# Kernel optimization log

Hardware: AMD Instinct MI355X
Metric: run time of the kernel (lower is better)

## Reference

```python
import jax, jax.numpy as jnp
import numpy as np

EPS = 1e-5
GROUPS = 8


def setup_inputs() -> dict:
    key = jax.random.key(0)
    ks = jax.random.split(key, 3)
    b, c, h, w = 8, 256, 64, 64
    x = jax.random.normal(ks[0], (b, c, h, w), dtype=jnp.float32)
    # 1x1 convs are just channel matmuls; store weights as [out_ch, in_ch]
    qkv_w = jax.random.normal(ks[1], (3 * c, c), dtype=jnp.float32) * (c ** -0.5)
    qkv_b = jnp.zeros((3 * c,), dtype=jnp.float32)
    out_w = jax.random.normal(ks[2], (c, c), dtype=jnp.float32) * (c ** -0.5)
    out_b = jnp.zeros((c,), dtype=jnp.float32)
    gn_w = jnp.ones((c,), dtype=jnp.float32)
    gn_b = jnp.zeros((c,), dtype=jnp.float32)
    return {"x": x, "gn_w": gn_w, "gn_b": gn_b, "qkv_w": qkv_w,
            "qkv_b": qkv_b, "out_w": out_w, "out_b": out_b}


def _group_norm(x, gn_w, gn_b):
    # x: [b, c, h, w]; normalize per (group, sample) over (c//g, h, w)
    b, c, h, w = x.shape
    xg = x.reshape(b, GROUPS, c // GROUPS, h * w)
    mean = xg.mean(axis=(2, 3), keepdims=True)
    var = xg.var(axis=(2, 3), keepdims=True)
    xn = (xg - mean) * jax.lax.rsqrt(var + EPS)
    xn = xn.reshape(b, c, h * w)
    return xn * gn_w[None, :, None] + gn_b[None, :, None]


def reference(x, gn_w, gn_b, qkv_w, qkv_b, out_w, out_b):
    b, c, h, w = x.shape
    scale = 1.0 / np.sqrt(c).astype(np.float32)  # matches channels ** -0.5
    nx = _group_norm(x, gn_w, gn_b)                       # [b, c, n]
    qkv = jnp.einsum('oc,bcn->bon', qkv_w, nx) + qkv_b[None, :, None]
    q, k, v = qkv[:, :c], qkv[:, c:2 * c], qkv[:, 2 * c:]  # each [b, c, n]
    attn = jnp.einsum('bci,bcj->bij', q, k) * scale        # [b, n, n]
    attn = jax.nn.softmax(attn, axis=-1)
    out = jnp.einsum('bij,bcj->bci', attn, v)              # [b, c, n]
    out = jnp.einsum('oc,bcn->bon', out_w, out) + out_b[None, :, None]
    return out.reshape(b, c, h, w) + x
```

## Files before the change

kernel.cpp:

```cpp
#include <hip/hip_runtime.h>
#include <math.h>


#define Bn 8
#define Cn 256
#define HWn 4096
#define Gn 8
#define CPGn 32
#define Mqkv 768
#define EPSf 1e-5f
#define QSCALEf 0.0625f
#define RTHR 8.0f

typedef short bf16x8 __attribute__((ext_vector_type(8)));
typedef float f32x4 __attribute__((ext_vector_type(4)));

__device__ __forceinline__ unsigned short f2bf(float f) {
  union { float f; unsigned u; } v; v.f = f;
  unsigned r = v.u + 0x7FFFu + ((v.u >> 16) & 1u);
  return (unsigned short)(r >> 16);
}

__device__ __forceinline__ int cvt_pk_bf16(float lo, float hi) {
  int d;
  asm("v_cvt_pk_bf16_f32 %0, %1, %2" : "=v"(d) : "v"(lo), "v"(hi));
  return d;
}

__global__ __launch_bounds__(1024)
void gn_stats_kernel(const float* __restrict__ x, const float* __restrict__ gn_w,
                     const float* __restrict__ gn_b, float* __restrict__ s_out,
                     float* __restrict__ t_out) {
  const int b = blockIdx.x / Gn, g = blockIdx.x % Gn;
  const float4* base = (const float4*)(x + ((size_t)(b * Cn + g * CPGn)) * HWn);
  const int n4 = CPGn * HWn / 4;
  float sum = 0.f, sq = 0.f;
  for (int i = threadIdx.x; i < n4; i += 1024) {
    float4 v = base[i];
    sum += (v.x + v.y) + (v.z + v.w);
    sq  += (v.x * v.x + v.y * v.y) + (v.z * v.z + v.w * v.w);
  }
  __shared__ float ss[1024], s2[1024];
  ss[threadIdx.x] = sum; s2[threadIdx.x] = sq;
  __syncthreads();
  for (int off = 512; off > 0; off >>= 1) {
    if ((int)threadIdx.x < off) {
      ss[threadIdx.x] += ss[threadIdx.x + off];
      s2[threadIdx.x] += s2[threadIdx.x + off];
    }
    __syncthreads();
  }
  if (threadIdx.x < CPGn) {
    const float inv_n = 1.f / (float)(CPGn * HWn);
    float mean = ss[0] * inv_n;
    float var  = s2[0] * inv_n - mean * mean;
    float rstd = rsqrtf(var + EPSf);
    int c = g * CPGn + (int)threadIdx.x;
    float sc = gn_w[c] * rstd;
    s_out[b * Cn + c] = sc;
    t_out[b * Cn + c] = gn_b[c] - mean * sc;
  }
}

__global__ __launch_bounds__(256)
void qkv_gemm_kernel(const float* __restrict__ x, const float* __restrict__ w,
                     const float* __restrict__ wb, const float* __restrict__ s_aff,
                     const float* __restrict__ t_aff, unsigned short* __restrict__ Qt,
                     unsigned short* __restrict__ Kt, unsigned short* __restrict__ Vb) {
  const int b = blockIdx.z;
  const int m0 = blockIdx.y * 64, n0 = blockIdx.x * 64;
  const int tid = threadIdx.x, tx = tid & 15, ty = tid >> 4;
  __shared__ float As[16][68];
  __shared__ float Bs[16][68];
  const float* xb = x + (size_t)b * Cn * HWn;
  const float* sb = s_aff + b * Cn;
  const float* tb = t_aff + b * Cn;
  float acc[4][4] = {};
  const int am = tid >> 2, ak = (tid & 3) * 4;
  const int bk = tid >> 4, bn = (tid & 15) * 4;
  for (int k0 = 0; k0 < Cn; k0 += 16) {
    {
      float4 a = *(const float4*)(w + (size_t)(m0 + am) * Cn + (k0 + ak));
      As[ak + 0][am] = a.x; As[ak + 1][am] = a.y; As[ak + 2][am] = a.z; As[ak + 3][am] = a.w;
      int c = k0 + bk;
      float4 v = *(const float4*)(xb + (size_t)c * HWn + (n0 + bn));
      float sc = sb[c], sh = tb[c];
      Bs[bk][bn + 0] = v.x * sc + sh; Bs[bk][bn + 1] = v.y * sc + sh;
      Bs[bk][bn + 2] = v.z * sc + sh; Bs[bk][bn + 3] = v.w * sc + sh;
    }
    __syncthreads();
#pragma unroll
    for (int kk = 0; kk < 16; ++kk) {
      float4 av = *(const float4*)&As[kk][ty * 4];
      float4 bv = *(const float4*)&Bs[kk][tx * 4];
      float aa[4] = {av.x, av.y, av.z, av.w};
      float bb[4] = {bv.x, bv.y, bv.z, bv.w};
#pragma unroll
      for (int i2 = 0; i2 < 4; ++i2)
#pragma unroll
        for (int j2 = 0; j2 < 4; ++j2)
          acc[i2][j2] = fmaf(aa[i2], bb[j2], acc[i2][j2]);
    }
    __syncthreads();
  }
  float bias[4];
#pragma unroll
  for (int i2 = 0; i2 < 4; ++i2) bias[i2] = wb[m0 + ty * 4 + i2];

  if (m0 < 512) {
    unsigned short* dst = (m0 < 256) ? Qt : Kt;
    const float scl = (m0 < 256) ? QSCALEf : 1.0f;
    const int cbase = (m0 & 255) + ty * 4;
#pragma unroll
    for (int j2 = 0; j2 < 4; ++j2) {
      int n = n0 + tx * 4 + j2;
      ushort4 pk;
      pk.x = f2bf((acc[0][j2] + bias[0]) * scl);
      pk.y = f2bf((acc[1][j2] + bias[1]) * scl);
      pk.z = f2bf((acc[2][j2] + bias[2]) * scl);
      pk.w = f2bf((acc[3][j2] + bias[3]) * scl);
      *(ushort4*)(dst + ((size_t)(b * HWn + n) * Cn + cbase)) = pk;
    }
  } else {
#pragma unroll
    for (int i2 = 0; i2 < 4; ++i2) {
      int c = (m0 - 512) + ty * 4 + i2;
      ushort4 pk;
      pk.x = f2bf(acc[i2][0] + bias[i2]);
      pk.y = f2bf(acc[i2][1] + bias[i2]);
      pk.z = f2bf(acc[i2][2] + bias[i2]);
      pk.w = f2bf(acc[i2][3] + bias[i2]);
      *(ushort4*)(Vb + ((size_t)(b * Cn + c) * HWn + n0 + tx * 4)) = pk;
    }
  }
}

__global__ __launch_bounds__(256, 2)
void attn_kernel(const unsigned short* __restrict__ Qt,
                 const unsigned short* __restrict__ Kt,
                 const unsigned short* __restrict__ Vb,
                 float* __restrict__ outp) {
  const int bid = blockIdx.x;
  const int b = bid & 7, i0 = (bid >> 3) * 64;
  const int tid = threadIdx.x;
  const int wv = tid >> 6, l = tid & 63;
  const int l15 = l & 15, lq = l >> 4;

  __shared__ unsigned short Ks[8192];
  __shared__ unsigned short Vs[8192];
  char* KsB = (char*)Ks;
  char* VsB = (char*)Vs;

  const unsigned short* Qb = Qt + ((size_t)b * HWn + i0) * Cn;
  const unsigned short* Kb = Kt + (size_t)b * HWn * Cn;
  const unsigned short* Vg = Vb + (size_t)b * Cn * HWn;

  bf16x8 qf[8];
  {
    const unsigned short* qrow = Qb + (size_t)(wv * 16 + l15) * Cn + lq * 8;
#pragma unroll
    for (int kc = 0; kc < 8; ++kc) qf[kc] = *(const bf16x8*)(qrow + kc * 32);
  }

  const int jk = ((tid >> 6) & 1) * 16 + (tid & 15);
  const int ck = (tid >> 7) * 32 + ((tid >> 4) & 3) * 8;
  const int cv = (tid >> 6) * 16 + (tid & 15);
  const int jv = ((tid >> 4) & 3) * 8;
  const unsigned short* gK = Kb + (size_t)jk * Cn + ck;
  const unsigned short* gV = Vg + (size_t)cv * HWn + jv;

  const int laneA = l15 + ((lq & 1) << 5);
  const int laneB = laneA + 16;
  const int shi = lq >> 1;

  bf16x8 kst[4], vst[4];
#pragma unroll
  for (int q = 0; q < 4; ++q) kst[q] = *(const bf16x8*)(gK + q * 64);
#pragma unroll
  for (int q = 0; q < 4; ++q) vst[q] = *(const bf16x8*)(gV + (size_t)q * 64 * HWn);
  gK += 32 * Cn; gV += 32;

  f32x4 o_acc[16];
#pragma unroll
  for (int cs = 0; cs < 16; ++cs) o_acc[cs] = (f32x4)(0.f);
  float m_i = -INFINITY, l_i = 0.f;

#pragma unroll 1
  for (int t = 0; t < 128; ++t) {
#pragma unroll
    for (int q = 0; q < 4; ++q) *(bf16x8*)(KsB + tid * 16 + q * 4096) = kst[q];
#pragma unroll
    for (int q = 0; q < 4; ++q) *(bf16x8*)(VsB + tid * 16 + q * 4096) = vst[q];
    __syncthreads();
    if (t < 127) {
#pragma unroll
      for (int q = 0; q < 4; ++q) kst[q] = *(const bf16x8*)(gK + q * 64);
#pragma unroll
      for (int q = 0; q < 4; ++q) vst[q] = *(const bf16x8*)(gV + (size_t)q * 64 * HWn);
      gK += 32 * Cn; gV += 32;
    }

    f32x4 s0 = (f32x4)(0.f), s1 = (f32x4)(0.f);
#pragma unroll
    for (int kc = 0; kc < 8; ++kc) {
      bf16x8 kf0 = *(const bf16x8*)(KsB + l * 16 + kc * 2048);
      bf16x8 kf1 = *(const bf16x8*)(KsB + l * 16 + kc * 2048 + 1024);
      s0 = __builtin_amdgcn_mfma_f32_16x16x32_bf16(kf0, qf[kc], s0, 0, 0, 0);
      s1 = __builtin_amdgcn_mfma_f32_16x16x32_bf16(kf1, qf[kc], s1, 0, 0, 0);
    }

    float p[2][4];
#pragma unroll
    for (int r = 0; r < 4; ++r) { p[0][r] = s0[r]; p[1][r] = s1[r]; }
    float rm = fmaxf(fmaxf(fmaxf(p[0][0], p[0][1]), fmaxf(p[0][2], p[0][3])),
                     fmaxf(fmaxf(p[1][0], p[1][1]), fmaxf(p[1][2], p[1][3])));
    rm = fmaxf(rm, __shfl_xor(rm, 16));
    rm = fmaxf(rm, __shfl_xor(rm, 32));
    if (!__all(rm - m_i <= RTHR)) {
      float mn = fmaxf(m_i, rm);
      float alpha = __expf(m_i - mn);
      m_i = mn;
      l_i *= alpha;
      float a0 = __shfl(alpha, 4 * lq + 0);
      float a1 = __shfl(alpha, 4 * lq + 1);
      float a2 = __shfl(alpha, 4 * lq + 2);
      float a3 = __shfl(alpha, 4 * lq + 3);
#pragma unroll
      for (int cs = 0; cs < 16; ++cs) {
        o_acc[cs][0] *= a0; o_acc[cs][1] *= a1;
        o_acc[cs][2] *= a2; o_acc[cs][3] *= a3;
      }
    }
    float rs = 0.f;
#pragma unroll
    for (int s = 0; s < 2; ++s)
#pragma unroll
      for (int r = 0; r < 4; ++r) { float e = __expf(p[s][r] - m_i); p[s][r] = e; rs += e; }
    rs += __shfl_xor(rs, 16);
    rs += __shfl_xor(rs, 32);
    l_i += rs;

    int d00 = cvt_pk_bf16(p[0][0], p[0][1]), d01 = cvt_pk_bf16(p[0][2], p[0][3]);
    int d10 = cvt_pk_bf16(p[1][0], p[1][1]), d11 = cvt_pk_bf16(p[1][2], p[1][3]);
    int A00 = __shfl(d00, laneA), A01 = __shfl(d01, laneA);
    int A10 = __shfl(d10, laneA), A11 = __shfl(d11, laneA);
    int B00 = __shfl(d00, laneB), B01 = __shfl(d01, laneB);
    int B10 = __shfl(d10, laneB), B11 = __shfl(d11, laneB);
    union { int w[4]; bf16x8 v; } pa;
    pa.w[0] = shi ? A10 : A00; pa.w[1] = shi ? A11 : A01;
    pa.w[2] = shi ? B10 : B00; pa.w[3] = shi ? B11 : B01;

#pragma unroll
    for (int cs = 0; cs < 16; ++cs) {
      bf16x8 vf = *(const bf16x8*)(VsB + l * 16 + cs * 1024);
      o_acc[cs] = __builtin_amdgcn_mfma_f32_16x16x32_bf16(pa.v, vf, o_acc[cs], 0, 0, 0);
    }
    __syncthreads();
  }

  float il = 1.f / l_i;
  float i0v = __shfl(il, 4 * lq + 0);
  float i1v = __shfl(il, 4 * lq + 1);
  float i2v = __shfl(il, 4 * lq + 2);
  float i3v = __shfl(il, 4 * lq + 3);
  float* ob = outp + (size_t)b * Cn * HWn;
  const int ibase = i0 + wv * 16 + lq * 4;
#pragma unroll
  for (int cs = 0; cs < 16; ++cs) {
    int c = cs * 16 + l15;
    float4 r4;
    r4.x = o_acc[cs][0] * i0v;
    r4.y = o_acc[cs][1] * i1v;
    r4.z = o_acc[cs][2] * i2v;
    r4.w = o_acc[cs][3] * i3v;
    *(float4*)(ob + (size_t)c * HWn + ibase) = r4;
  }
}

__global__ __launch_bounds__(256)
void out_gemm_kernel(const float* __restrict__ tmp, const float* __restrict__ w,
                     const float* __restrict__ wb, const float* __restrict__ xres,
                     float* __restrict__ y) {
  const int b = blockIdx.z;
  const int m0 = blockIdx.y * 64, n0 = blockIdx.x * 64;
  const int tid = threadIdx.x, tx = tid & 15, ty = tid >> 4;
  __shared__ float As[16][68];
  __shared__ float Bs[16][68];
  const float* tb = tmp + (size_t)b * Cn * HWn;
  float acc[4][4] = {};
  const int am = tid >> 2, ak = (tid & 3) * 4;
  const int bk = tid >> 4, bn = (tid & 15) * 4;
  for (int k0 = 0; k0 < Cn; k0 += 16) {
    {
      float4 a = *(const float4*)(w + (size_t)(m0 + am) * Cn + (k0 + ak));
      As[ak + 0][am] = a.x; As[ak + 1][am] = a.y; As[ak + 2][am] = a.z; As[ak + 3][am] = a.w;
      int c = k0 + bk;
      float4 vv = *(const float4*)(tb + (size_t)c * HWn + (n0 + bn));
      Bs[bk][bn + 0] = vv.x; Bs[bk][bn + 1] = vv.y; Bs[bk][bn + 2] = vv.z; Bs[bk][bn + 3] = vv.w;
    }
    __syncthreads();
#pragma unroll
    for (int kk = 0; kk < 16; ++kk) {
      float4 av = *(const float4*)&As[kk][ty * 4];
      float4 bv = *(const float4*)&Bs[kk][tx * 4];
      float aa[4] = {av.x, av.y, av.z, av.w};
      float bb[4] = {bv.x, bv.y, bv.z, bv.w};
#pragma unroll
      for (int i2 = 0; i2 < 4; ++i2)
#pragma unroll
        for (int j2 = 0; j2 < 4; ++j2)
          acc[i2][j2] = fmaf(aa[i2], bb[j2], acc[i2][j2]);
    }
    __syncthreads();
  }
  float* yb = y + (size_t)b * Cn * HWn;
  const float* xb = xres + (size_t)b * Cn * HWn;
#pragma unroll
  for (int i2 = 0; i2 < 4; ++i2) {
    int m = m0 + ty * 4 + i2;
    float bias = wb[m];
    float4 xr = *(const float4*)(xb + (size_t)m * HWn + n0 + tx * 4);
    float4 r;
    r.x = acc[i2][0] + bias + xr.x; r.y = acc[i2][1] + bias + xr.y;
    r.z = acc[i2][2] + bias + xr.z; r.w = acc[i2][3] + bias + xr.w;
    *(float4*)(yb + (size_t)m * HWn + n0 + tx * 4) = r;
  }
}

extern "C" void kernel_launch(void* const* d_in, const int* in_sizes, int n_in,
                              void* d_out, int out_size, void* d_ws, size_t ws_size,
                              hipStream_t stream) {
  (void)in_sizes; (void)n_in; (void)out_size; (void)ws_size;
  const float* x     = (const float*)d_in[0];
  const float* gn_w  = (const float*)d_in[1];
  const float* gn_b  = (const float*)d_in[2];
  const float* qkv_w = (const float*)d_in[3];
  const float* qkv_b = (const float*)d_in[4];
  const float* out_w = (const float*)d_in[5];
  const float* out_b = (const float*)d_in[6];
  float* out = (float*)d_out;

  char* ws = (char*)d_ws;
  float* s_aff = (float*)ws;
  float* t_aff = s_aff + Bn * Cn;
  unsigned short* Qt = (unsigned short*)(ws + 16384);
  unsigned short* Kt = Qt + (size_t)Bn * HWn * Cn;
  unsigned short* Vb = Kt + (size_t)Bn * HWn * Cn;
  float* tmp = (float*)(Vb + (size_t)Bn * HWn * Cn);

  gn_stats_kernel<<<dim3(Bn * Gn), 1024, 0, stream>>>(x, gn_w, gn_b, s_aff, t_aff);
  qkv_gemm_kernel<<<dim3(64, 12, Bn), 256, 0, stream>>>(x, qkv_w, qkv_b, s_aff, t_aff, Qt, Kt, Vb);
  attn_kernel<<<dim3(512), 256, 0, stream>>>(Qt, Kt, Vb, tmp);
  out_gemm_kernel<<<dim3(64, 4, Bn), 256, 0, stream>>>(tmp, out_w, out_b, x, out);
}
```

Measured before the change: 482.1 us.

## Move QKV and output projections to bf16 MFMA with transposed bf16 activations

```diff
diff --git a/kernel.cpp b/kernel.cpp
--- a/kernel.cpp
+++ b/kernel.cpp
@@ -63,74 +63,127 @@
 }
 
 __global__ __launch_bounds__(256)
-void qkv_gemm_kernel(const float* __restrict__ x, const float* __restrict__ w,
-                     const float* __restrict__ wb, const float* __restrict__ s_aff,
-                     const float* __restrict__ t_aff, unsigned short* __restrict__ Qt,
+void affine_transpose_kernel(const float* __restrict__ x, const float* __restrict__ s_aff,
+                             const float* __restrict__ t_aff, unsigned short* __restrict__ nxT) {
+  const int bid = blockIdx.x;
+  const int b = bid & 7, r = bid >> 3;
+  const int c0 = (r & 3) * 64, n0 = (r >> 2) * 64;
+  const int tid = threadIdx.x;
+  __shared__ unsigned int ld32[64][33];
+  const float* xb = x + ((size_t)(b * Cn + c0)) * HWn + n0;
+  const int cl0 = tid >> 4, nn = (tid & 15) * 4;
+#pragma unroll
+  for (int it = 0; it < 4; ++it) {
+    int cl = cl0 + 16 * it;
+    int c = c0 + cl;
+    float sc = s_aff[b * Cn + c], sh = t_aff[b * Cn + c];
+    float4 v = *(const float4*)(xb + (size_t)cl * HWn + nn);
+    ld32[cl][(nn >> 1) + 0] = (unsigned)cvt_pk_bf16(v.x * sc + sh, v.y * sc + sh);
+    ld32[cl][(nn >> 1) + 1] = (unsigned)cvt_pk_bf16(v.z * sc + sh, v.w * sc + sh);
+  }
+  __syncthreads();
+#pragma unroll
+  for (int it = 0; it < 2; ++it) {
+    int chunk = tid + 256 * it;
+    int n = chunk >> 3, cg = chunk & 7;
+    union { unsigned short u[8]; bf16x8 v; } o;
+#pragma unroll
+    for (int k = 0; k < 8; ++k) {
+      unsigned w32 = ld32[cg * 8 + k][n >> 1];
+      o.u[k] = (unsigned short)((n & 1) ? (w32 >> 16) : (w32 & 0xffffu));
+    }
+    *(bf16x8*)(nxT + ((size_t)(b * HWn + n0 + n)) * Cn + c0 + cg * 8) = o.v;
+  }
+}
+
+__global__ __launch_bounds__(256, 2)
+void qkv_gemm_kernel(const unsigned short* __restrict__ nxT, const float* __restrict__ w,
+                     const float* __restrict__ wb, unsigned short* __restrict__ Qt,
                      unsigned short* __restrict__ Kt, unsigned short* __restrict__ Vb) {
-  const int b = blockIdx.z;
-  const int m0 = blockIdx.y * 64, n0 = blockIdx.x * 64;
-  const int tid = threadIdx.x, tx = tid & 15, ty = tid >> 4;
-  __shared__ float As[16][68];
-  __shared__ float Bs[16][68];
-  const float* xb = x + (size_t)b * Cn * HWn;
-  const float* sb = s_aff + b * Cn;
-  const float* tb = t_aff + b * Cn;
-  float acc[4][4] = {};
-  const int am = tid >> 2, ak = (tid & 3) * 4;
-  const int bk = tid >> 4, bn = (tid & 15) * 4;
-  for (int k0 = 0; k0 < Cn; k0 += 16) {
-    {
-      float4 a = *(const float4*)(w + (size_t)(m0 + am) * Cn + (k0 + ak));
-      As[ak + 0][am] = a.x; As[ak + 1][am] = a.y; As[ak + 2][am] = a.z; As[ak + 3][am] = a.w;
-      int c = k0 + bk;
-      float4 v = *(const float4*)(xb + (size_t)c * HWn + (n0 + bn));
-      float sc = sb[c], sh = tb[c];
-      Bs[bk][bn + 0] = v.x * sc + sh; Bs[bk][bn + 1] = v.y * sc + sh;
-      Bs[bk][bn + 2] = v.z * sc + sh; Bs[bk][bn + 3] = v.w * sc + sh;
-    }
-    __syncthreads();
-#pragma unroll
-    for (int kk = 0; kk < 16; ++kk) {
-      float4 av = *(const float4*)&As[kk][ty * 4];
-      float4 bv = *(const float4*)&Bs[kk][tx * 4];
-      float aa[4] = {av.x, av.y, av.z, av.w};
-      float bb[4] = {bv.x, bv.y, bv.z, bv.w};
-#pragma unroll
-      for (int i2 = 0; i2 < 4; ++i2)
-#pragma unroll
-        for (int j2 = 0; j2 < 4; ++j2)
-          acc[i2][j2] = fmaf(aa[i2], bb[j2], acc[i2][j2]);
-    }
-    __syncthreads();
-  }
-  float bias[4];
-#pragma unroll
-  for (int i2 = 0; i2 < 4; ++i2) bias[i2] = wb[m0 + ty * 4 + i2];
-
-  if (m0 < 512) {
+  const int bid = blockIdx.x;
+  const int b = bid & 7, r = bid >> 3;
+  const int n0 = (r & 63) * 64, m0 = (r >> 6) * 128;
+  const int tid = threadIdx.x;
+  const int wv = tid >> 6, l = tid & 63;
+  const int l15 = l & 15, lq = l >> 4;
+  const int ob = m0 + wv * 32;
+
+  bf16x8 wf[2][8];
+#pragma unroll
+  for (int g = 0; g < 2; ++g) {
+    const float* wr = w + (size_t)(ob + g * 16 + l15) * Cn + lq * 8;
+#pragma unroll
+    for (int kc = 0; kc < 8; ++kc) {
+      float4 a = *(const float4*)(wr + kc * 32);
+      float4 c4 = *(const float4*)(wr + kc * 32 + 4);
+      union { int w4[4]; bf16x8 v; } u;
+      u.w4[0] = cvt_pk_bf16(a.x, a.y);  u.w4[1] = cvt_pk_bf16(a.z, a.w);
+      u.w4[2] = cvt_pk_bf16(c4.x, c4.y); u.w4[3] = cvt_pk_bf16(c4.z, c4.w);
+      wf[g][kc] = u.v;
+    }
+  }
+
+  const unsigned short* nb = nxT + (size_t)b * HWn * Cn + lq * 8;
+  f32x4 acc[2][4];
+#pragma unroll
+  for (int g = 0; g < 2; ++g)
+#pragma unroll
+    for (int s = 0; s < 4; ++s) acc[g][s] = (f32x4)(0.f);
+
+  const bool isV = (m0 >= 512);
+#pragma unroll
+  for (int s = 0; s < 4; ++s) {
+    const unsigned short* np = nb + (size_t)(n0 + s * 16 + l15) * Cn;
+#pragma unroll
+    for (int kc = 0; kc < 8; ++kc) {
+      bf16x8 xf = *(const bf16x8*)(np + kc * 32);
+      if (!isV) {
+        acc[0][s] = __builtin_amdgcn_mfma_f32_16x16x32_bf16(wf[0][kc], xf, acc[0][s], 0, 0, 0);
+        acc[1][s] = __builtin_amdgcn_mfma_f32_16x16x32_bf16(wf[1][kc], xf, acc[1][s], 0, 0, 0);
+      } else {
+        acc[0][s] = __builtin_amdgcn_mfma_f32_16x16x32_bf16(xf, wf[0][kc], acc[0][s], 0, 0, 0);
+        acc[1][s] = __builtin_amdgcn_mfma_f32_16x16x32_bf16(xf, wf[1][kc], acc[1][s], 0, 0, 0);
+      }
+    }
+  }
+
+  if (!isV) {
     unsigned short* dst = (m0 < 256) ? Qt : Kt;
     const float scl = (m0 < 256) ? QSCALEf : 1.0f;
-    const int cbase = (m0 & 255) + ty * 4;
-#pragma unroll
-    for (int j2 = 0; j2 < 4; ++j2) {
-      int n = n0 + tx * 4 + j2;
-      ushort4 pk;
-      pk.x = f2bf((acc[0][j2] + bias[0]) * scl);
-      pk.y = f2bf((acc[1][j2] + bias[1]) * scl);
-      pk.z = f2bf((acc[2][j2] + bias[2]) * scl);
-      pk.w = f2bf((acc[3][j2] + bias[3]) * scl);
-      *(ushort4*)(dst + ((size_t)(b * HWn + n) * Cn + cbase)) = pk;
+#pragma unroll
+    for (int g = 0; g < 2; ++g) {
+      int cb = ((ob + g * 16) & 255) + lq * 4;
+      float b0 = wb[ob + g * 16 + lq * 4 + 0];
+      float b1 = wb[ob + g * 16 + lq * 4 + 1];
+      float b2 = wb[ob + g * 16 + lq * 4 + 2];
+      float b3 = wb[ob + g * 16 + lq * 4 + 3];
+#pragma unroll
+      for (int s = 0; s < 4; ++s) {
+        int n = n0 + s * 16 + l15;
+        ushort4 pk;
+        pk.x = f2bf((acc[g][s][0] + b0) * scl);
+        pk.y = f2bf((acc[g][s][1] + b1) * scl);
+        pk.z = f2bf((acc[g][s][2] + b2) * scl);
+        pk.w = f2bf((acc[g][s][3] + b3) * scl);
+        *(ushort4*)(dst + ((size_t)(b * HWn + n)) * Cn + cb) = pk;
+      }
     }
   } else {
 #pragma unroll
-    for (int i2 = 0; i2 < 4; ++i2) {
-      int c = (m0 - 512) + ty * 4 + i2;
-      ushort4 pk;
-      pk.x = f2bf(acc[i2][0] + bias[i2]);
-      pk.y = f2bf(acc[i2][1] + bias[i2]);
-      pk.z = f2bf(acc[i2][2] + bias[i2]);
-      pk.w = f2bf(acc[i2][3] + bias[i2]);
-      *(ushort4*)(Vb + ((size_t)(b * Cn + c) * HWn + n0 + tx * 4)) = pk;
+    for (int g = 0; g < 2; ++g) {
+      int o = ob + g * 16 + l15;
+      int c = o - 512;
+      float bias = wb[o];
+#pragma unroll
+      for (int s = 0; s < 4; ++s) {
+        int n = n0 + s * 16 + lq * 4;
+        ushort4 pk;
+        pk.x = f2bf(acc[g][s][0] + bias);
+        pk.y = f2bf(acc[g][s][1] + bias);
+        pk.z = f2bf(acc[g][s][2] + bias);
+        pk.w = f2bf(acc[g][s][3] + bias);
+        *(ushort4*)(Vb + ((size_t)(b * Cn + c)) * HWn + n) = pk;
+      }
     }
   }
 }
@@ -139,7 +192,7 @@
 void attn_kernel(const unsigned short* __restrict__ Qt,
                  const unsigned short* __restrict__ Kt,
                  const unsigned short* __restrict__ Vb,
-                 float* __restrict__ outp) {
+                 unsigned short* __restrict__ outp) {
   const int bid = blockIdx.x;
   const int b = bid & 7, i0 = (bid >> 3) * 64;
   const int tid = threadIdx.x;
@@ -211,7 +264,7 @@
 
     float p[2][4];
 #pragma unroll
-    for (int r = 0; r < 4; ++r) { p[0][r] = s0[r]; p[1][r] = s1[r]; }
+    for (int u = 0; u < 4; ++u) { p[0][u] = s0[u]; p[1][u] = s1[u]; }
     float rm = fmaxf(fmaxf(fmaxf(p[0][0], p[0][1]), fmaxf(p[0][2], p[0][3])),
                      fmaxf(fmaxf(p[1][0], p[1][1]), fmaxf(p[1][2], p[1][3])));
     rm = fmaxf(rm, __shfl_xor(rm, 16));
@@ -235,7 +288,7 @@
 #pragma unroll
     for (int s = 0; s < 2; ++s)
 #pragma unroll
-      for (int r = 0; r < 4; ++r) { float e = __expf(p[s][r] - m_i); p[s][r] = e; rs += e; }
+      for (int u = 0; u < 4; ++u) { float e = __expf(p[s][u] - m_i); p[s][u] = e; rs += e; }
     rs += __shfl_xor(rs, 16);
     rs += __shfl_xor(rs, 32);
     l_i += rs;
@@ -263,67 +316,79 @@
   float i1v = __shfl(il, 4 * lq + 1);
   float i2v = __shfl(il, 4 * lq + 2);
   float i3v = __shfl(il, 4 * lq + 3);
-  float* ob = outp + (size_t)b * Cn * HWn;
+  unsigned short* ob = outp + (size_t)b * HWn * Cn;
   const int ibase = i0 + wv * 16 + lq * 4;
 #pragma unroll
   for (int cs = 0; cs < 16; ++cs) {
     int c = cs * 16 + l15;
-    float4 r4;
-    r4.x = o_acc[cs][0] * i0v;
-    r4.y = o_acc[cs][1] * i1v;
-    r4.z = o_acc[cs][2] * i2v;
-    r4.w = o_acc[cs][3] * i3v;
-    *(float4*)(ob + (size_t)c * HWn + ibase) = r4;
-  }
-}
-
-__global__ __launch_bounds__(256)
-void out_gemm_kernel(const float* __restrict__ tmp, const float* __restrict__ w,
+    ob[(size_t)(ibase + 0) * Cn + c] = f2bf(o_acc[cs][0] * i0v);
+    ob[(size_t)(ibase + 1) * Cn + c] = f2bf(o_acc[cs][1] * i1v);
+    ob[(size_t)(ibase + 2) * Cn + c] = f2bf(o_acc[cs][2] * i2v);
+    ob[(size_t)(ibase + 3) * Cn + c] = f2bf(o_acc[cs][3] * i3v);
+  }
+}
+
+__global__ __launch_bounds__(256, 2)
+void out_gemm_kernel(const unsigned short* __restrict__ tmpT, const float* __restrict__ w,
                      const float* __restrict__ wb, const float* __restrict__ xres,
                      float* __restrict__ y) {
-  const int b = blockIdx.z;
-  const int m0 = blockIdx.y * 64, n0 = blockIdx.x * 64;
-  const int tid = threadIdx.x, tx = tid & 15, ty = tid >> 4;
-  __shared__ float As[16][68];
-  __shared__ float Bs[16][68];
-  const float* tb = tmp + (size_t)b * Cn * HWn;
-  float acc[4][4] = {};
-  const int am = tid >> 2, ak = (tid & 3) * 4;
-  const int bk = tid >> 4, bn = (tid & 15) * 4;
-  for (int k0 = 0; k0 < Cn; k0 += 16) {
-    {
-      float4 a = *(const float4*)(w + (size_t)(m0 + am) * Cn + (k0 + ak));
-      As[ak + 0][am] = a.x; As[ak + 1][am] = a.y; As[ak + 2][am] = a.z; As[ak + 3][am] = a.w;
-      int c = k0 + bk;
-      float4 vv = *(const float4*)(tb + (size_t)c * HWn + (n0 + bn));
-      Bs[bk][bn + 0] = vv.x; Bs[bk][bn + 1] = vv.y; Bs[bk][bn + 2] = vv.z; Bs[bk][bn + 3] = vv.w;
-    }
-    __syncthreads();
-#pragma unroll
-    for (int kk = 0; kk < 16; ++kk) {
-      float4 av = *(const float4*)&As[kk][ty * 4];
-      float4 bv = *(const float4*)&Bs[kk][tx * 4];
-      float aa[4] = {av.x, av.y, av.z, av.w};
-      float bb[4] = {bv.x, bv.y, bv.z, bv.w};
-#pragma unroll
-      for (int i2 = 0; i2 < 4; ++i2)
-#pragma unroll
-        for (int j2 = 0; j2 < 4; ++j2)
-          acc[i2][j2] = fmaf(aa[i2], bb[j2], acc[i2][j2]);
-    }
-    __syncthreads();
-  }
-  float* yb = y + (size_t)b * Cn * HWn;
-  const float* xb = xres + (size_t)b * Cn * HWn;
-#pragma unroll
-  for (int i2 = 0; i2 < 4; ++i2) {
-    int m = m0 + ty * 4 + i2;
-    float bias = wb[m];
-    float4 xr = *(const float4*)(xb + (size_t)m * HWn + n0 + tx * 4);
-    float4 r;
-    r.x = acc[i2][0] + bias + xr.x; r.y = acc[i2][1] + bias + xr.y;
-    r.z = acc[i2][2] + bias + xr.z; r.w = acc[i2][3] + bias + xr.w;
-    *(float4*)(yb + (size_t)m * HWn + n0 + tx * 4) = r;
+  const int bid = blockIdx.x;
+  const int b = bid & 7, r = bid >> 3;
+  const int n0 = (r & 63) * 64, m0 = (r >> 6) * 128;
+  const int tid = threadIdx.x;
+  const int wv = tid >> 6, l = tid & 63;
+  const int l15 = l & 15, lq = l >> 4;
+  const int ob = m0 + wv * 32;
+
+  bf16x8 wf[2][8];
+#pragma unroll
+  for (int g = 0; g < 2; ++g) {
+    const float* wr = w + (size_t)(ob + g * 16 + l15) * Cn + lq * 8;
+#pragma unroll
+    for (int kc = 0; kc < 8; ++kc) {
+      float4 a = *(const float4*)(wr + kc * 32);
+      float4 c4 = *(const float4*)(wr + kc * 32 + 4);
+      union { int w4[4]; bf16x8 v; } u;
+      u.w4[0] = cvt_pk_bf16(a.x, a.y);  u.w4[1] = cvt_pk_bf16(a.z, a.w);
+      u.w4[2] = cvt_pk_bf16(c4.x, c4.y); u.w4[3] = cvt_pk_bf16(c4.z, c4.w);
+      wf[g][kc] = u.v;
+    }
+  }
+
+  const unsigned short* tb = tmpT + (size_t)b * HWn * Cn + lq * 8;
+  f32x4 acc[2][4];
+#pragma unroll
+  for (int g = 0; g < 2; ++g)
+#pragma unroll
+    for (int s = 0; s < 4; ++s) acc[g][s] = (f32x4)(0.f);
+
+#pragma unroll
+  for (int s = 0; s < 4; ++s) {
+    const unsigned short* tp = tb + (size_t)(n0 + s * 16 + l15) * Cn;
+#pragma unroll
+    for (int kc = 0; kc < 8; ++kc) {
+      bf16x8 tf = *(const bf16x8*)(tp + kc * 32);
+      acc[0][s] = __builtin_amdgcn_mfma_f32_16x16x32_bf16(tf, wf[0][kc], acc[0][s], 0, 0, 0);
+      acc[1][s] = __builtin_amdgcn_mfma_f32_16x16x32_bf16(tf, wf[1][kc], acc[1][s], 0, 0, 0);
+    }
+  }
+
+#pragma unroll
+  for (int g = 0; g < 2; ++g) {
+    int o = ob + g * 16 + l15;
+    float bias = wb[o];
+#pragma unroll
+    for (int s = 0; s < 4; ++s) {
+      int n = n0 + s * 16 + lq * 4;
+      size_t idx = ((size_t)(b * Cn + o)) * HWn + n;
+      float4 xr = *(const float4*)(xres + idx);
+      float4 out;
+      out.x = acc[g][s][0] + bias + xr.x;
+      out.y = acc[g][s][1] + bias + xr.y;
+      out.z = acc[g][s][2] + bias + xr.z;
+      out.w = acc[g][s][3] + bias + xr.w;
+      *(float4*)(y + idx) = out;
+    }
   }
 }
 
@@ -343,13 +408,15 @@
   char* ws = (char*)d_ws;
   float* s_aff = (float*)ws;
   float* t_aff = s_aff + Bn * Cn;
-  unsigned short* Qt = (unsigned short*)(ws + 16384);
-  unsigned short* Kt = Qt + (size_t)Bn * HWn * Cn;
-  unsigned short* Vb = Kt + (size_t)Bn * HWn * Cn;
-  float* tmp = (float*)(Vb + (size_t)Bn * HWn * Cn);
+  unsigned short* Qt  = (unsigned short*)(ws + 16384);
+  unsigned short* Kt  = Qt  + (size_t)Bn * HWn * Cn;
+  unsigned short* Vb  = Kt  + (size_t)Bn * HWn * Cn;
+  unsigned short* nxT = Vb  + (size_t)Bn * HWn * Cn;
+  unsigned short* tmpT = nxT + (size_t)Bn * HWn * Cn;
 
   gn_stats_kernel<<<dim3(Bn * Gn), 1024, 0, stream>>>(x, gn_w, gn_b, s_aff, t_aff);
-  qkv_gemm_kernel<<<dim3(64, 12, Bn), 256, 0, stream>>>(x, qkv_w, qkv_b, s_aff, t_aff, Qt, Kt, Vb);
-  attn_kernel<<<dim3(512), 256, 0, stream>>>(Qt, Kt, Vb, tmp);
-  out_gemm_kernel<<<dim3(64, 4, Bn), 256, 0, stream>>>(tmp, out_w, out_b, x, out);
-}
+  affine_transpose_kernel<<<dim3(2048), 256, 0, stream>>>(x, s_aff, t_aff, nxT);
+  qkv_gemm_kernel<<<dim3(3072), 256, 0, stream>>>(nxT, qkv_w, qkv_b, Qt, Kt, Vb);
+  attn_kernel<<<dim3(512), 256, 0, stream>>>(Qt, Kt, Vb, tmpT);
+  out_gemm_kernel<<<dim3(1024), 256, 0, stream>>>(tmpT, out_w, out_b, x, out);
+}
```

Result: faster. 397.2 us (median of 2 runs) (-17.6%).
